# Kernel optimization log

Hardware: AMD Instinct MI355X
Metric: run time of the kernel (lower is better)

The kernel has to match this reference:

```python
import jax, jax.numpy as jnp
import numpy as np

N = 50000       # nodes
E = 800000      # edges
F_IN = 128      # dataset.num_node_features
H = 128         # hidden_channels (all equal), pool_dim
FC1, FC2 = 512, 256
G = 512         # number of graphs
C = 32          # dataset.num_classes
EPS = 1e-5      # BatchNorm eps


def setup_inputs() -> dict:
    key = jax.random.key(0)
    ks = jax.random.split(key, 16)
    rn = lambda k, s: jax.random.normal(k, s, jnp.float32) * 0.05
    return {
        "x": jax.random.normal(ks[0], (N, F_IN), jnp.float32),
        "edge_index": jax.random.randint(ks[1], (2, E), 0, N),
        "batch": jnp.sort(jax.random.randint(ks[2], (N,), 0, G)),
        "W1": rn(ks[3], (F_IN, H)), "b1": jnp.zeros((H,), jnp.float32),
        "W2": rn(ks[4], (H, H)),    "b2": jnp.zeros((H,), jnp.float32),
        "W3": rn(ks[5], (H, H)),    "b3": jnp.zeros((H,), jnp.float32),
        "W4": rn(ks[6], (H, H)),    "b4": jnp.zeros((H,), jnp.float32),
        "lw1": rn(ks[7], (H, FC1)),   "lb1": jnp.zeros((FC1,), jnp.float32),
        "lw2": rn(ks[8], (FC1, FC2)), "lb2": jnp.zeros((FC2,), jnp.float32),
        "lw3": rn(ks[9], (FC2, C)),   "lb3": jnp.zeros((C,), jnp.float32),
        "g1": jnp.ones((FC1,), jnp.float32), "be1": jnp.zeros((FC1,), jnp.float32),
        "g2": jnp.ones((FC2,), jnp.float32), "be2": jnp.zeros((FC2,), jnp.float32),
    }


def _gcn_structure(edge_index):
    # add self loops, then symmetric deg^-1/2 normalization (PyG GCNConv default)
    loop = jnp.arange(N)
    src = jnp.concatenate([edge_index[0], loop])
    dst = jnp.concatenate([edge_index[1], loop])
    deg = jax.ops.segment_sum(jnp.ones_like(src, jnp.float32), dst, num_segments=N)
    dinv = jnp.where(deg > 0, jax.lax.rsqrt(deg), 0.0)
    norm = dinv[src] * dinv[dst]          # [E + N]
    return src, dst, norm


def _gcn_conv(x, src, dst, norm, W, b):
    h = x @ W                              # [N, out]
    agg = jax.ops.segment_sum(h[src] * norm[:, None], dst, num_segments=N)
    return agg + b


def _bn(h, gamma, beta):
    # training-mode batch stats (biased variance), as torch BatchNorm1d
    m = jnp.mean(h, axis=0)
    v = jnp.var(h, axis=0)
    return (h - m) * jax.lax.rsqrt(v + EPS) * gamma + beta


def reference(x, edge_index, batch, W1, b1, W2, b2, W3, b3, W4, b4,
              lw1, lb1, lw2, lb2, lw3, lb3, g1, be1, g2, be2):
    src, dst, norm = _gcn_structure(edge_index)
    x = jax.nn.relu(_gcn_conv(x, src, dst, norm, W1, b1))
    x = jax.nn.relu(_gcn_conv(x, src, dst, norm, W2, b2))
    x = jax.nn.relu(_gcn_conv(x, src, dst, norm, W3, b3))
    x = jax.nn.relu(_gcn_conv(x, src, dst, norm, W4, b4))
    # global_add_pool over graphs
    p = jax.ops.segment_sum(x, batch, num_segments=G)   # [G, H]
    h = jax.nn.relu(p @ lw1 + lb1)
    h = _bn(h, g1, be1)                                  # dropout = identity (eval)
    h = jax.nn.relu(h @ lw2 + lb2)
    h = _bn(h, g2, be2)
    return jax.nn.sigmoid(h @ lw3 + lb3)                 # [G, C]
```

## Files before the change

kernel.cpp:

```cpp
#include <hip/hip_runtime.h>
#include <hip/hip_fp16.h>
#include <math.h>

#define NN 50000
#define NE 800000
#define FT 128
#define NG 512
#define F1 512
#define F2 256
#define NC 32
#define BN_EPS 1e-5f

typedef __attribute__((ext_vector_type(8))) unsigned short ushort8;
typedef __attribute__((ext_vector_type(8))) _Float16 f16x8;
typedef __attribute__((ext_vector_type(4))) float f32x4;

__device__ __forceinline__ unsigned short f2h(float f) {
  return __half_as_ushort(__float2half(f));
}
__device__ __forceinline__ float h2f(unsigned short h) {
  return __half2float(__ushort_as_half(h));
}


__global__ __launch_bounds__(256) void k_hist(const int* __restrict__ ei, int* __restrict__ cnt) {
  int e = blockIdx.x * 256 + threadIdx.x;
  if (e < NE) atomicAdd(&cnt[ei[NE + e]], 1);
}

__global__ __launch_bounds__(256) void k_dinv(const int* __restrict__ cnt, float* __restrict__ dinv) {
  int i = blockIdx.x * 256 + threadIdx.x;
  if (i < NN) dinv[i] = rsqrtf((float)(cnt[i] + 1));
}

__global__ __launch_bounds__(256) void k_scan1(const int* __restrict__ cnt, int* __restrict__ bsum) {
  __shared__ int s[256];
  int t = threadIdx.x, i = blockIdx.x * 256 + t;
  s[t] = (i < NN) ? cnt[i] : 0;
  __syncthreads();
  for (int d = 128; d > 0; d >>= 1) {
    if (t < d) s[t] += s[t + d];
    __syncthreads();
  }
  if (t == 0) bsum[blockIdx.x] = s[0];
}

__global__ __launch_bounds__(256) void k_scan2(const int* __restrict__ bsum, int* __restrict__ bscan, int nb) {
  __shared__ int s[256];
  int t = threadIdx.x;
  int v = (t < nb) ? bsum[t] : 0;
  s[t] = v; __syncthreads();
  for (int d = 1; d < 256; d <<= 1) {
    int a = (t >= d) ? s[t - d] : 0;
    __syncthreads();
    s[t] += a;
    __syncthreads();
  }
  bscan[t] = s[t] - v;
}

__global__ __launch_bounds__(256) void k_scan3(const int* __restrict__ cnt, const int* __restrict__ bscan,
                                               int* __restrict__ off) {
  __shared__ int s[256];
  int t = threadIdx.x, i = blockIdx.x * 256 + t;
  int v = (i < NN) ? cnt[i] : 0;
  s[t] = v; __syncthreads();
  for (int d = 1; d < 256; d <<= 1) {
    int a = (t >= d) ? s[t - d] : 0;
    __syncthreads();
    s[t] += a;
    __syncthreads();
  }
  int base = bscan[blockIdx.x];
  if (i < NN) off[i] = base + s[t] - v;
  if (i == NN - 1) off[NN] = base + s[t];
}

__global__ __launch_bounds__(256) void k_fill(const int* __restrict__ ei, const int* __restrict__ off,
                                              int* __restrict__ cur, const float* __restrict__ dinv,
                                              unsigned int* __restrict__ ep) {
  int e = blockIdx.x * 256 + threadIdx.x;
  if (e >= NE) return;
  int s = ei[e], d = ei[NE + e];
  int p = off[d] + atomicAdd(&cur[d], 1);
  float w = dinv[s] * dinv[d];
  ep[p] = (unsigned int)(s & 0xFFFF) | ((unsigned int)f2h(w) << 16);
}


__global__ __launch_bounds__(256) void k_wprep(const float* __restrict__ W, unsigned short* __restrict__ Wt) {
  int idx = blockIdx.x * 256 + threadIdx.x;
  int c = idx >> 7, k = idx & 127;
  int byte = c * 256 + k * 2;
  byte ^= (c & 7) << 4;
  Wt[byte >> 1] = f2h(W[k * FT + c]);
}


template <int FIRST>
__global__ __launch_bounds__(256) void k_gemm_mfma(const float* __restrict__ Xf,
                                                   const unsigned short* __restrict__ Xh,
                                                   const unsigned short* __restrict__ Wt,
                                                   unsigned short* __restrict__ Oc) {
  __shared__ unsigned short sA[64 * 128];
  __shared__ unsigned short sB[128 * 128];
  int t = threadIdx.x;
#pragma unroll
  for (int i = 0; i < 8; ++i) {
    int off = t * 16 + i * 4096;
    *(float4*)((char*)sB + off) = *(const float4*)((const char*)Wt + off);
  }
  {
    int row = t >> 2, k0 = (t & 3) * 32;
    int grow = blockIdx.x * 64 + row;
    if (grow >= NN) grow = NN - 1;
    if (FIRST) {
      const float* xr = Xf + (size_t)grow * FT + k0;
#pragma unroll
      for (int j = 0; j < 4; ++j) {
        float4 v0 = *(const float4*)&xr[j * 8];
        float4 v1 = *(const float4*)&xr[j * 8 + 4];
        ushort8 w;
        w[0] = f2h(v0.x); w[1] = f2h(v0.y); w[2] = f2h(v0.z); w[3] = f2h(v0.w);
        w[4] = f2h(v1.x); w[5] = f2h(v1.y); w[6] = f2h(v1.z); w[7] = f2h(v1.w);
        int byte = row * 256 + (k0 + j * 8) * 2;
        byte ^= (row & 7) << 4;
        *(ushort8*)((char*)sA + byte) = w;
      }
    } else {
#pragma unroll
      for (int j = 0; j < 4; ++j) {
        int k = k0 + j * 8;
        int ch = k >> 5, ko = k & 31;
        ushort8 v = *(const ushort8*)&Xh[((size_t)ch * NN + grow) * 32 + ko];
        int byte = row * 256 + k * 2;
        byte ^= (row & 7) << 4;
        *(ushort8*)((char*)sA + byte) = v;
      }
    }
  }
  __syncthreads();
  int w = t >> 6, l = t & 63;
  int m = l & 15, ks = l >> 4;
  f16x8 a[4];
#pragma unroll
  for (int kk = 0; kk < 4; ++kk) {
    int r = w * 16 + m;
    int byte = r * 256 + (kk * 32 + ks * 8) * 2;
    byte ^= (r & 7) << 4;
    a[kk] = *(const f16x8*)((const char*)sA + byte);
  }
  f32x4 acc[8];
#pragma unroll
  for (int nf = 0; nf < 8; ++nf) acc[nf] = (f32x4){0.f, 0.f, 0.f, 0.f};
#pragma unroll
  for (int nf = 0; nf < 8; ++nf) {
#pragma unroll
    for (int kk = 0; kk < 4; ++kk) {
      int col = nf * 16 + m;
      int byte = col * 256 + (kk * 32 + ks * 8) * 2;
      byte ^= (col & 7) << 4;
      f16x8 b = *(const f16x8*)((const char*)sB + byte);
      acc[nf] = __builtin_amdgcn_mfma_f32_16x16x32_f16(a[kk], b, acc[nf], 0, 0, 0);
    }
  }
  int orow0 = blockIdx.x * 64 + w * 16 + ks * 4;
#pragma unroll
  for (int nf = 0; nf < 8; ++nf) {
    int ch = nf >> 1;
    int co = ((nf & 1) << 4) + m;
#pragma unroll
    for (int r = 0; r < 4; ++r) {
      int orow = orow0 + r;
      if (orow < NN) Oc[((size_t)ch * NN + orow) * 32 + co] = f2h(acc[nf][r]);
    }
  }
}


__global__ __launch_bounds__(256) void k_aggc(const unsigned short* __restrict__ Hc,
                                              const float* __restrict__ dinv,
                                              const int* __restrict__ off, const unsigned int* __restrict__ ep,
                                              const float* __restrict__ bias, unsigned short* __restrict__ O) {
  int c = blockIdx.x & 3;
  int grp = blockIdx.x >> 2;
  int t = threadIdx.x;
  int node = grp * 64 + (t >> 2);
  int l = t & 3;
  if (node >= NN) return;
  const unsigned short* base = Hc + (size_t)c * NN * 32 + l * 8;
  float di = dinv[node];
  float sw = di * di;
  float acc[8];
  {
    ushort8 sv = *(const ushort8*)&base[(size_t)node * 32];
#pragma unroll
    for (int i = 0; i < 8; ++i) acc[i] = h2f(sv[i]) * sw;
  }
  int e0 = off[node], e1 = off[node + 1];
  int e = e0;
  for (; e + 8 <= e1; e += 8) {
    unsigned int pw[8];
#pragma unroll
    for (int j = 0; j < 8; ++j) pw[j] = ep[e + j];
    ushort8 v[8];
#pragma unroll
    for (int j = 0; j < 8; ++j) v[j] = *(const ushort8*)&base[(size_t)(pw[j] & 0xFFFFu) * 32];
#pragma unroll
    for (int j = 0; j < 8; ++j) {
      float w = h2f((unsigned short)(pw[j] >> 16));
#pragma unroll
      for (int i = 0; i < 8; ++i) acc[i] += h2f(v[j][i]) * w;
    }
  }
  for (; e + 4 <= e1; e += 4) {
    unsigned int p0 = ep[e], p1 = ep[e + 1], p2 = ep[e + 2], p3 = ep[e + 3];
    ushort8 v0 = *(const ushort8*)&base[(size_t)(p0 & 0xFFFFu) * 32];
    ushort8 v1 = *(const ushort8*)&base[(size_t)(p1 & 0xFFFFu) * 32];
    ushort8 v2 = *(const ushort8*)&base[(size_t)(p2 & 0xFFFFu) * 32];
    ushort8 v3 = *(const ushort8*)&base[(size_t)(p3 & 0xFFFFu) * 32];
    float w0 = h2f((unsigned short)(p0 >> 16));
    float w1 = h2f((unsigned short)(p1 >> 16));
    float w2 = h2f((unsigned short)(p2 >> 16));
    float w3 = h2f((unsigned short)(p3 >> 16));
#pragma unroll
    for (int i = 0; i < 8; ++i) acc[i] += h2f(v0[i]) * w0;
#pragma unroll
    for (int i = 0; i < 8; ++i) acc[i] += h2f(v1[i]) * w1;
#pragma unroll
    for (int i = 0; i < 8; ++i) acc[i] += h2f(v2[i]) * w2;
#pragma unroll
    for (int i = 0; i < 8; ++i) acc[i] += h2f(v3[i]) * w3;
  }
  for (; e < e1; ++e) {
    unsigned int pv = ep[e];
    float w = h2f((unsigned short)(pv >> 16));
    ushort8 v = *(const ushort8*)&base[(size_t)(pv & 0xFFFFu) * 32];
#pragma unroll
    for (int i = 0; i < 8; ++i) acc[i] += h2f(v[i]) * w;
  }
  ushort8 outv;
#pragma unroll
  for (int i = 0; i < 8; ++i) {
    float v = acc[i] + bias[c * 32 + l * 8 + i];
    outv[i] = f2h(fmaxf(v, 0.f));
  }
  *(ushort8*)&O[((size_t)c * NN + node) * 32 + l * 8] = outv;
}


__global__ __launch_bounds__(256) void k_bounds(const int* __restrict__ batch, int* __restrict__ gstart,
                                                int* __restrict__ gend) {
  int i = blockIdx.x * 256 + threadIdx.x;
  if (i >= NN) return;
  int b = batch[i];
  if (i == 0 || batch[i - 1] != b) gstart[b] = i;
  if (i == NN - 1 || batch[i + 1] != b) gend[b] = i + 1;
}

__global__ __launch_bounds__(128) void k_pool(const unsigned short* __restrict__ X, const int* __restrict__ gstart,
                                              const int* __restrict__ gend, float* __restrict__ pool) {
  int g = blockIdx.x, t = threadIdx.x;
  int ch = t >> 5, wo = t & 31;
  float s = 0.f;
  int n0 = gstart[g], n1 = gend[g];
  const unsigned short* base = X + (size_t)ch * NN * 32 + wo;
  for (int n = n0; n < n1; ++n) s += h2f(base[(size_t)n * 32]);
  pool[g * FT + t] = s;
}


__global__ __launch_bounds__(256) void k_fc1(const float* __restrict__ P, const float* __restrict__ W,
                                             const float* __restrict__ B, float* __restrict__ O) {
  __shared__ float sp[FT];
  int g = blockIdx.x, t = threadIdx.x;
  if (t < FT) sp[t] = P[g * FT + t];
  __syncthreads();
  float a0 = B[t], a1 = B[t + 256];
  for (int k = 0; k < FT; ++k) {
    float x = sp[k];
    a0 += x * W[k * F1 + t];
    a1 += x * W[k * F1 + t + 256];
  }
  O[g * F1 + t] = fmaxf(a0, 0.f);
  O[g * F1 + t + 256] = fmaxf(a1, 0.f);
}

__global__ __launch_bounds__(256) void k_bnstats(const float* __restrict__ h, int cols,
                                                 float* __restrict__ bm, float* __restrict__ br) {
  __shared__ float ss[256], s2[256];
  int c = blockIdx.x, t = threadIdx.x;
  float a = 0.f, b = 0.f;
  for (int r = t; r < NG; r += 256) {
    float v = h[r * cols + c];
    a += v; b += v * v;
  }
  ss[t] = a; s2[t] = b; __syncthreads();
  for (int d = 128; d > 0; d >>= 1) {
    if (t < d) { ss[t] += ss[t + d]; s2[t] += s2[t + d]; }
    __syncthreads();
  }
  if (t == 0) {
    float m = ss[0] / NG;
    float var = s2[0] / NG - m * m;
    bm[c] = m;
    br[c] = rsqrtf(var + BN_EPS);
  }
}

__global__ __launch_bounds__(256) void k_fc2(const float* __restrict__ H1, const float* __restrict__ bm,
                                             const float* __restrict__ br, const float* __restrict__ gam,
                                             const float* __restrict__ bet, const float* __restrict__ W,
                                             const float* __restrict__ B, float* __restrict__ O) {
  __shared__ float sh[F1];
  int g = blockIdx.x, t = threadIdx.x;
  for (int k = t; k < F1; k += 256) {
    float v = H1[g * F1 + k];
    sh[k] = (v - bm[k]) * br[k] * gam[k] + bet[k];
  }
  __syncthreads();
  float a = B[t];
  for (int k = 0; k < F1; ++k) a += sh[k] * W[k * F2 + t];
  O[g * F2 + t] = fmaxf(a, 0.f);
}

__global__ __launch_bounds__(256) void k_fc3(const float* __restrict__ H2, const float* __restrict__ bm,
                                             const float* __restrict__ br, const float* __restrict__ gam,
                                             const float* __restrict__ bet, const float* __restrict__ W,
                                             const float* __restrict__ B, float* __restrict__ O) {
  __shared__ float sh[F2];
  int g = blockIdx.x, t = threadIdx.x;
  if (t < F2) {
    float v = H2[g * F2 + t];
    sh[t] = (v - bm[t]) * br[t] * gam[t] + bet[t];
  }
  __syncthreads();
  if (t < NC) {
    float a = B[t];
    for (int k = 0; k < F2; ++k) a += sh[k] * W[k * NC + t];
    O[g * NC + t] = 1.f / (1.f + expf(-a));
  }
}


extern "C" void kernel_launch(void* const* d_in, const int* in_sizes, int n_in,
                              void* d_out, int out_size, void* d_ws, size_t ws_size,
                              hipStream_t stream) {
  const float* x     = (const float*)d_in[0];
  const int*   ei    = (const int*)d_in[1];
  const int*   batch = (const int*)d_in[2];
  const float* Wc[4] = {(const float*)d_in[3], (const float*)d_in[5], (const float*)d_in[7], (const float*)d_in[9]};
  const float* Bc[4] = {(const float*)d_in[4], (const float*)d_in[6], (const float*)d_in[8], (const float*)d_in[10]};
  const float* lw1 = (const float*)d_in[11]; const float* lb1 = (const float*)d_in[12];
  const float* lw2 = (const float*)d_in[13]; const float* lb2 = (const float*)d_in[14];
  const float* lw3 = (const float*)d_in[15]; const float* lb3 = (const float*)d_in[16];
  const float* g1  = (const float*)d_in[17]; const float* be1 = (const float*)d_in[18];
  const float* g2  = (const float*)d_in[19]; const float* be2 = (const float*)d_in[20];

  char* p = (char*)d_ws;
  auto take = [&](size_t bytes) {
    char* r = p;
    p += (bytes + 255) & ~(size_t)255;
    return r;
  };
  int*   cnt    = (int*)take((size_t)NN * 4);
  float* dinv   = (float*)take((size_t)NN * 4);
  int*   off    = (int*)take((size_t)(NN + 1) * 4);
  int*   cur    = (int*)take((size_t)NN * 4);
  int*   bsum   = (int*)take(256 * 4);
  int*   bscan  = (int*)take(256 * 4);
  int*   gstart = (int*)take((size_t)NG * 4);
  int*   gend   = (int*)take((size_t)NG * 4);
  unsigned int*   ep   = (unsigned int*)take((size_t)NE * 4);
  unsigned short* Wt   = (unsigned short*)take((size_t)FT * FT * 2);
  unsigned short* bufT = (unsigned short*)take((size_t)NN * FT * 2);
  unsigned short* bufA = (unsigned short*)take((size_t)NN * FT * 2);
  unsigned short* bufB = (unsigned short*)take((size_t)NN * FT * 2);
  float* pool   = (float*)take((size_t)NG * FT * 4);
  float* h1     = (float*)take((size_t)NG * F1 * 4);
  float* h2     = (float*)take((size_t)NG * F2 * 4);
  float* bnm1   = (float*)take(F1 * 4);
  float* bnr1   = (float*)take(F1 * 4);
  float* bnm2   = (float*)take(F2 * 4);
  float* bnr2   = (float*)take(F2 * 4);

  const int NB = (NN + 255) / 256;

  hipMemsetAsync(cnt, 0, (size_t)NN * 4, stream);
  hipMemsetAsync(cur, 0, (size_t)NN * 4, stream);
  hipMemsetAsync(gstart, 0, (size_t)NG * 4, stream);
  hipMemsetAsync(gend, 0, (size_t)NG * 4, stream);

  k_hist<<<NE / 256, 256, 0, stream>>>(ei, cnt);
  k_dinv<<<NB, 256, 0, stream>>>(cnt, dinv);
  k_scan1<<<NB, 256, 0, stream>>>(cnt, bsum);
  k_scan2<<<1, 256, 0, stream>>>(bsum, bscan, NB);
  k_scan3<<<NB, 256, 0, stream>>>(cnt, bscan, off);
  k_fill<<<NE / 256, 256, 0, stream>>>(ei, off, cur, dinv, ep);

  const int NBLK_G = (NN + 63) / 64;
  const int NGRP_A = (NN + 63) / 64;
  unsigned short* outs[4] = {bufA, bufB, bufA, bufB};
  for (int l = 0; l < 4; ++l) {
    k_wprep<<<64, 256, 0, stream>>>(Wc[l], Wt);
    if (l == 0)
      k_gemm_mfma<1><<<NBLK_G, 256, 0, stream>>>(x, (const unsigned short*)nullptr, Wt, bufT);
    else
      k_gemm_mfma<0><<<NBLK_G, 256, 0, stream>>>((const float*)nullptr, outs[l - 1], Wt, bufT);
    k_aggc<<<NGRP_A * 4, 256, 0, stream>>>(bufT, dinv, off, ep, Bc[l], outs[l]);
  }

  k_bounds<<<NB, 256, 0, stream>>>(batch, gstart, gend);
  k_pool<<<NG, 128, 0, stream>>>(bufB, gstart, gend, pool);

  k_fc1<<<NG, 256, 0, stream>>>(pool, lw1, lb1, h1);
  k_bnstats<<<F1, 256, 0, stream>>>(h1, F1, bnm1, bnr1);
  k_fc2<<<NG, 256, 0, stream>>>(h1, bnm1, bnr1, g1, be1, lw2, lb2, h2);
  k_bnstats<<<F2, 256, 0, stream>>>(h2, F2, bnm2, bnr2);
  k_fc3<<<NG, 256, 0, stream>>>(h2, bnm2, bnr2, g2, be2, lw3, lb3, (float*)d_out);
}
```

Measured before the change: 343.3 us.

## Partition edge histogram/fill by destination slice and degree-sort aggregation nodes

The histogram and CSR fill kernels now read eight destinations per thread with vector loads. Each edge chunk is processed by eight blocks, and each block only does atomics for destinations in its own slice of the node range, which is meant to localize atomic traffic. A degree-bucket permutation is also built (histogram, scan, scatter), and the aggregation kernel walks nodes in degree order so that threads in a wavefront see similar edge counts, reducing divergence and load imbalance. The cost is eightfold redundant reads of the edge list, three extra small kernels, and nondeterministic node order within buckets, which may hurt locality of output writes.

```diff
diff --git a/kernel.cpp b/kernel.cpp
--- a/kernel.cpp
+++ b/kernel.cpp
@@ -10,6 +10,7 @@
 #define F2 256
 #define NC 32
 #define BN_EPS 1e-5f
+#define NSLC (NN / 8)
 
 typedef __attribute__((ext_vector_type(8))) unsigned short ushort8;
 typedef __attribute__((ext_vector_type(8))) _Float16 f16x8;
@@ -24,8 +25,17 @@
 
 
 __global__ __launch_bounds__(256) void k_hist(const int* __restrict__ ei, int* __restrict__ cnt) {
-  int e = blockIdx.x * 256 + threadIdx.x;
-  if (e < NE) atomicAdd(&cnt[ei[NE + e]], 1);
+  int c = blockIdx.x & 7;
+  int lo = c * NSLC, hi = lo + NSLC;
+  int e0 = (blockIdx.x >> 3) * 2048 + threadIdx.x * 8;
+  if (e0 >= NE) return;
+  const int* dst = ei + NE;
+  int4 a = *(const int4*)&dst[e0];
+  int4 b = *(const int4*)&dst[e0 + 4];
+  int d[8] = {a.x, a.y, a.z, a.w, b.x, b.y, b.z, b.w};
+#pragma unroll
+  for (int j = 0; j < 8; ++j)
+    if (d[j] >= lo && d[j] < hi) atomicAdd(&cnt[d[j]], 1);
 }
 
 __global__ __launch_bounds__(256) void k_dinv(const int* __restrict__ cnt, float* __restrict__ dinv) {
@@ -79,12 +89,53 @@
 __global__ __launch_bounds__(256) void k_fill(const int* __restrict__ ei, const int* __restrict__ off,
                                               int* __restrict__ cur, const float* __restrict__ dinv,
                                               unsigned int* __restrict__ ep) {
-  int e = blockIdx.x * 256 + threadIdx.x;
-  if (e >= NE) return;
-  int s = ei[e], d = ei[NE + e];
-  int p = off[d] + atomicAdd(&cur[d], 1);
-  float w = dinv[s] * dinv[d];
-  ep[p] = (unsigned int)(s & 0xFFFF) | ((unsigned int)f2h(w) << 16);
+  int c = blockIdx.x & 7;
+  int lo = c * NSLC, hi = lo + NSLC;
+  int e0 = (blockIdx.x >> 3) * 2048 + threadIdx.x * 8;
+  if (e0 >= NE) return;
+  const int* dst = ei + NE;
+  int4 da = *(const int4*)&dst[e0];
+  int4 db = *(const int4*)&dst[e0 + 4];
+  int4 sa = *(const int4*)&ei[e0];
+  int4 sb = *(const int4*)&ei[e0 + 4];
+  int d[8] = {da.x, da.y, da.z, da.w, db.x, db.y, db.z, db.w};
+  int s[8] = {sa.x, sa.y, sa.z, sa.w, sb.x, sb.y, sb.z, sb.w};
+#pragma unroll
+  for (int j = 0; j < 8; ++j) {
+    if (d[j] >= lo && d[j] < hi) {
+      float w = dinv[s[j]] * dinv[d[j]];
+      int p = off[d[j]] + atomicAdd(&cur[d[j]], 1);
+      ep[p] = (unsigned int)(s[j] & 0xFFFF) | ((unsigned int)f2h(w) << 16);
+    }
+  }
+}
+
+
+__global__ __launch_bounds__(256) void k_dhist(const int* __restrict__ cnt, int* __restrict__ dh) {
+  int i = blockIdx.x * 256 + threadIdx.x;
+  if (i < NN) atomicAdd(&dh[min(cnt[i], 63)], 1);
+}
+
+__global__ __launch_bounds__(64) void k_dscan(const int* __restrict__ dh, int* __restrict__ doff) {
+  __shared__ int s[64];
+  int t = threadIdx.x;
+  int v = dh[t];
+  s[t] = v; __syncthreads();
+  for (int d = 1; d < 64; d <<= 1) {
+    int a = (t >= d) ? s[t - d] : 0;
+    __syncthreads();
+    s[t] += a;
+    __syncthreads();
+  }
+  doff[t] = s[t] - v;
+}
+
+__global__ __launch_bounds__(256) void k_dscatter(const int* __restrict__ cnt, const int* __restrict__ doff,
+                                                  int* __restrict__ dcur, int* __restrict__ perm) {
+  int i = blockIdx.x * 256 + threadIdx.x;
+  if (i >= NN) return;
+  int b = min(cnt[i], 63);
+  perm[doff[b] + atomicAdd(&dcur[b], 1)] = i;
 }
 
 
@@ -181,13 +232,15 @@
 __global__ __launch_bounds__(256) void k_aggc(const unsigned short* __restrict__ Hc,
                                               const float* __restrict__ dinv,
                                               const int* __restrict__ off, const unsigned int* __restrict__ ep,
+                                              const int* __restrict__ perm,
                                               const float* __restrict__ bias, unsigned short* __restrict__ O) {
   int c = blockIdx.x & 3;
   int grp = blockIdx.x >> 2;
   int t = threadIdx.x;
-  int node = grp * 64 + (t >> 2);
+  int idx = grp * 64 + (t >> 2);
   int l = t & 3;
-  if (node >= NN) return;
+  if (idx >= NN) return;
+  int node = perm[idx];
   const unsigned short* base = Hc + (size_t)c * NN * 32 + l * 8;
   float di = dinv[node];
   float sw = di * di;
@@ -371,6 +424,10 @@
   int*   bscan  = (int*)take(256 * 4);
   int*   gstart = (int*)take((size_t)NG * 4);
   int*   gend   = (int*)take((size_t)NG * 4);
+  int*   dh     = (int*)take(64 * 4);
+  int*   doff   = (int*)take(64 * 4);
+  int*   dcur   = (int*)take(64 * 4);
+  int*   perm   = (int*)take((size_t)NN * 4);
   unsigned int*   ep   = (unsigned int*)take((size_t)NE * 4);
   unsigned short* Wt   = (unsigned short*)take((size_t)FT * FT * 2);
   unsigned short* bufT = (unsigned short*)take((size_t)NN * FT * 2);
@@ -390,13 +447,19 @@
   hipMemsetAsync(cur, 0, (size_t)NN * 4, stream);
   hipMemsetAsync(gstart, 0, (size_t)NG * 4, stream);
   hipMemsetAsync(gend, 0, (size_t)NG * 4, stream);
-
-  k_hist<<<NE / 256, 256, 0, stream>>>(ei, cnt);
+  hipMemsetAsync(dh, 0, 64 * 4, stream);
+  hipMemsetAsync(dcur, 0, 64 * 4, stream);
+
+  const int NB_EX = ((NE + 2047) / 2048) * 8;
+  k_hist<<<NB_EX, 256, 0, stream>>>(ei, cnt);
   k_dinv<<<NB, 256, 0, stream>>>(cnt, dinv);
   k_scan1<<<NB, 256, 0, stream>>>(cnt, bsum);
   k_scan2<<<1, 256, 0, stream>>>(bsum, bscan, NB);
   k_scan3<<<NB, 256, 0, stream>>>(cnt, bscan, off);
-  k_fill<<<NE / 256, 256, 0, stream>>>(ei, off, cur, dinv, ep);
+  k_fill<<<NB_EX, 256, 0, stream>>>(ei, off, cur, dinv, ep);
+  k_dhist<<<NB, 256, 0, stream>>>(cnt, dh);
+  k_dscan<<<1, 64, 0, stream>>>(dh, doff);
+  k_dscatter<<<NB, 256, 0, stream>>>(cnt, doff, dcur, perm);
 
   const int NBLK_G = (NN + 63) / 64;
   const int NGRP_A = (NN + 63) / 64;
@@ -407,7 +470,7 @@
       k_gemm_mfma<1><<<NBLK_G, 256, 0, stream>>>(x, (const unsigned short*)nullptr, Wt, bufT);
     else
       k_gemm_mfma<0><<<NBLK_G, 256, 0, stream>>>((const float*)nullptr, outs[l - 1], Wt, bufT);
-    k_aggc<<<NGRP_A * 4, 256, 0, stream>>>(bufT, dinv, off, ep, Bc[l], outs[l]);
+    k_aggc<<<NGRP_A * 4, 256, 0, stream>>>(bufT, dinv, off, ep, perm, Bc[l], outs[l]);
   }
 
   k_bounds<<<NB, 256, 0, stream>>>(batch, gstart, gend);
```

Result: slower. 631.9 us (+84.1%).
